# Kernel optimization log

Hardware: AMD Instinct MI355X
Metric: run time of the kernel (lower is better)

Reference implementation:

```python
import jax, jax.numpy as jnp
import numpy as np

B, T, I, H, C = 128, 512, 256, 512, 4


def setup_inputs() -> dict:
    key = jax.random.key(0)
    ks = jax.random.split(key, 11)
    s = lambda fan_in: 1.0 / np.sqrt(fan_in)
    return {
        "x": jax.random.normal(ks[0], (B, T, I), dtype=jnp.float32),
        "W_x1": jax.random.uniform(ks[1], (I, 4 * H), jnp.float32, -s(I), s(I)),
        "b_x1": jax.random.uniform(ks[2], (4 * H,), jnp.float32, -s(I), s(I)),
        "W_h1": jax.random.uniform(ks[3], (H, 4 * H), jnp.float32, -s(H), s(H)),
        "b_h1": jax.random.uniform(ks[4], (4 * H,), jnp.float32, -s(H), s(H)),
        "W_x2": jax.random.uniform(ks[5], (H, 4 * H), jnp.float32, -s(H), s(H)),
        "b_x2": jax.random.uniform(ks[6], (4 * H,), jnp.float32, -s(H), s(H)),
        "W_h2": jax.random.uniform(ks[7], (H, 4 * H), jnp.float32, -s(H), s(H)),
        "b_h2": jax.random.uniform(ks[8], (4 * H,), jnp.float32, -s(H), s(H)),
        "W_head": jax.random.uniform(ks[9], (H, C), jnp.float32, -s(H), s(H)),
        "b_head": jax.random.uniform(ks[10], (C,), jnp.float32, -s(H), s(H)),
    }


def _lstm_layer(x_proj_seq, W_h, b_h, hidden):
    """x_proj_seq: [T, B, 4H] precomputed input projection (incl. x bias).
    Returns full hidden sequence [T, B, H] and final (h, c)."""
    def step(carry, xp_t):
        h, c = carry
        gates = xp_t + h @ W_h + b_h  # [B, 4H]
        i_t, f_t, g_t, o_t = jnp.split(gates, 4, axis=-1)
        i_t = jax.nn.sigmoid(i_t)
        f_t = jax.nn.sigmoid(f_t)
        g_t = jnp.tanh(g_t)
        o_t = jax.nn.sigmoid(o_t)
        c_t = f_t * c + i_t * g_t
        h_t = o_t * jnp.tanh(c_t)
        return (h_t, c_t), h_t

    batch = x_proj_seq.shape[1]
    init = (jnp.zeros((batch, hidden), x_proj_seq.dtype),
            jnp.zeros((batch, hidden), x_proj_seq.dtype))
    (h_T, c_T), h_seq = jax.lax.scan(step, init, x_proj_seq)
    return h_seq, h_T


def reference(x, W_x1, b_x1, W_h1, b_h1, W_x2, b_x2, W_h2, b_h2, W_head, b_head):
    H_ = W_h1.shape[0]
    # Precompute input projections for all timesteps as one big GEMM per layer.
    xp1 = jnp.einsum('bti,ig->tbg', x, W_x1) + b_x1  # [T, B, 4H]
    h1_seq, _ = _lstm_layer(xp1, W_h1, b_h1, H_)      # [T, B, H]
    xp2 = jnp.einsum('tbh,hg->tbg', h1_seq, W_x2) + b_x2
    _, h2_T = _lstm_layer(xp2, W_h2, b_h2, H_)        # [B, H]
    return h2_T @ W_head + b_head                     # [B, C]
```

## Files before the change

### kernel.cpp

```cpp
#include <hip/hip_runtime.h>
#include <cstddef>

#define Bb 128
#define Tt 512
#define Ii 256
#define Hh 512
#define G4c 2048
#define BHc (Bb * Hh)
#define FSTRIDE 32

typedef float    f32x4 __attribute__((ext_vector_type(4)));
typedef _Float16 f16x8 __attribute__((ext_vector_type(8)));
typedef unsigned int u32x4 __attribute__((ext_vector_type(4)));

#define OFF_WT1 0u
#define OFF_WT2 3145728u
#define OFF_BC1 7340032u
#define OFF_BC2 7348224u
#define OFF_H1  7356416u
#define OFF_H2  7749632u
#define OFF_FLG 8011776u
#define OFF_END 8028160u

__device__ __forceinline__ float sigm(float x)  { return 1.0f / (1.0f + __expf(-x)); }
__device__ __forceinline__ float tanhf_(float x){ return 1.0f - 2.0f / (1.0f + __expf(2.0f * x)); }

__device__ __forceinline__ void ld_g_f16x8_sc(f16x8& dst, const _Float16* p) {
  asm volatile("global_load_dwordx4 %0, %1, off sc0 sc1"
               : "=v"(dst) : "v"(p) : "memory");
}
__device__ __forceinline__ void ld_g_f32x4(f32x4& dst, const float* p) {
  asm volatile("global_load_dwordx4 %0, %1, off" : "=v"(dst) : "v"(p) : "memory");
}
__device__ __forceinline__ void st_g_f16_sc(_Float16* p, _Float16 v) {
  unsigned u = (unsigned)__builtin_bit_cast(unsigned short, v);
  asm volatile("global_store_short %0, %1, off sc0 sc1" :: "v"(p), "v"(u) : "memory");
}
__device__ __forceinline__ void wait_vm0() {
  asm volatile("s_waitcnt vmcnt(0)" ::: "memory");
}

__device__ __forceinline__ void poll2(unsigned* base, int tid,
                                      unsigned tgtA, unsigned tgtB) {
  if (tid < 64) {
    const unsigned tgt = (tid < 32) ? tgtA : tgtB;
    unsigned* p = base + (size_t)tid * FSTRIDE;
    unsigned v;
    do {
      v = __hip_atomic_load(p, __ATOMIC_RELAXED, __HIP_MEMORY_SCOPE_AGENT);
    } while (__any(v < tgt));
  }
  __syncthreads();
}

__device__ __forceinline__ void publish(unsigned* myflag, int tid, unsigned val) {
  wait_vm0();
  __syncthreads();
  if (tid == 0)
    __hip_atomic_store(myflag, val, __ATOMIC_RELAXED, __HIP_MEMORY_SCOPE_AGENT);
}

__global__ void init_weights(const float* __restrict__ Wx1, const float* __restrict__ Wh1,
                             const float* __restrict__ bx1, const float* __restrict__ bh1,
                             const float* __restrict__ Wx2, const float* __restrict__ Wh2,
                             const float* __restrict__ bx2, const float* __restrict__ bh2,
                             _Float16* __restrict__ Wt1, _Float16* __restrict__ Wt2,
                             float* __restrict__ bc1, float* __restrict__ bc2) {
  const int b = blockIdx.x;
  const int layer = b >> 11;
  const int jb = (b >> 6) & 31;
  const int ln = b & 63;
  const int t  = threadIdx.x;
  const int ks = t >> 3;
  const int i  = t & 7;
  const int k  = (ks << 5) + ((ln >> 4) << 3) + i;
  if (layer == 0) {
    if (ln == 0 && t < 16) {
      #pragma unroll
      for (int g = 0; g < 4; ++g) {
        const int gc = (g << 9) + (jb << 4) + t;
        bc1[gc] = bx1[gc] + bh1[gc];
      }
    }
    if (ks < 24) {
      #pragma unroll
      for (int g = 0; g < 4; ++g) {
        const int gc = (g << 9) + (jb << 4) + (ln & 15);
        const float v = (k < Ii) ? Wx1[k * G4c + gc] : Wh1[(k - Ii) * G4c + gc];
        Wt1[((((size_t)jb * 24 + ks) * 4 + g) * 64 + ln) * 8 + i] = (_Float16)v;
      }
    }
  } else {
    if (ln == 0 && t < 16) {
      #pragma unroll
      for (int g = 0; g < 4; ++g) {
        const int gc = (g << 9) + (jb << 4) + t;
        bc2[gc] = bx2[gc] + bh2[gc];
      }
    }
    #pragma unroll
    for (int g = 0; g < 4; ++g) {
      const int gc = (g << 9) + (jb << 4) + (ln & 15);
      const float v = (k < Hh) ? Wx2[k * G4c + gc] : Wh2[(k - Hh) * G4c + gc];
      Wt2[((((size_t)jb * 32 + ks) * 4 + g) * 64 + ln) * 8 + i] = (_Float16)v;
    }
  }
}

__global__ void zero_ws(u32x4* p, int n) {
  const int i = blockIdx.x * blockDim.x + threadIdx.x;
  if (i < n) p[i] = (u32x4){0u, 0u, 0u, 0u};
}

__global__ __launch_bounds__(256, 1) void lstm_main(
    const float* __restrict__ x,
    const _Float16* __restrict__ Wt1, const _Float16* __restrict__ Wt2,
    const float* __restrict__ bc1, const float* __restrict__ bc2,
    _Float16* h1buf, _Float16* h2buf, unsigned* flags,
    const float* __restrict__ Whead, const float* __restrict__ bhead,
    float* __restrict__ out)
{
  extern __shared__ char smem[];

  const int tid  = threadIdx.x;
  const int lane = tid & 63;
  const int wv   = tid >> 6;
  const int bid  = blockIdx.x;
  const int layer = bid >> 6;
  const int blkL  = bid & 63;
  const int jb = blkL >> 1;
  const int rh = blkL & 1;
  const int j0 = jb << 4;

  unsigned* grp = flags + (size_t)(rh << 6) * FSTRIDE;
  unsigned* myflag = grp + (size_t)((layer << 5) + jb) * FSTRIDE;

  {
    const int elems16 = layer ? (131072 / 16) : (98304 / 16);
    const u32x4* src = (const u32x4*)((layer ? Wt2 : Wt1)
                                      + (size_t)jb * (layer ? 65536 : 49152));
    u32x4* dst = (u32x4*)smem;
    for (int i = tid; i < elems16; i += 256) dst[i] = src[i];
  }
  __syncthreads();

  const int c15 = lane & 15;
  const int kg  = lane >> 4;
  const int arow  = (rh << 6) + (wv << 4) + c15;
  const int wrow0 = (rh << 6) + (wv << 4) + (kg << 2);

  const float* bc = layer ? bc2 : bc1;
  const float bias0 = bc[        j0 + c15];
  const float bias1 = bc[ 512 +  j0 + c15];
  const float bias2 = bc[1024 +  j0 + c15];
  const float bias3 = bc[1536 +  j0 + c15];

  const int lb = lane << 4;

  f32x4 cst = {0.f, 0.f, 0.f, 0.f};

  int m3w = 0;
  int m3r = 2;

  for (int e = 0; e <= Tt; ++e) {
    if (layer == 0) {
      if (e >= Tt) break;
      f32x4 xf[16];
      const float* xp = x + (size_t)arow * (Tt * Ii) + (size_t)e * Ii + (kg << 3);
      #pragma unroll
      for (int ks = 0; ks < 8; ++ks) {
        ld_g_f32x4(xf[2*ks],   xp + (ks << 5));
        ld_g_f32x4(xf[2*ks+1], xp + (ks << 5) + 4);
      }
      poll2(grp, tid, (unsigned)e, e ? (unsigned)(e - 1) : 0u);
      f16x8 af[24];
      const _Float16* hp = h1buf + (size_t)m3r * BHc + arow * Hh + (kg << 3);
      #pragma unroll
      for (int ks = 0; ks < 16; ++ks)
        ld_g_f16x8_sc(af[8 + ks], hp + (ks << 5));
      wait_vm0();
      __builtin_amdgcn_sched_barrier(0);
      #pragma unroll
      for (int ks = 0; ks < 8; ++ks) {
        f16x8 v;
        v[0] = (_Float16)xf[2*ks][0]; v[1] = (_Float16)xf[2*ks][1];
        v[2] = (_Float16)xf[2*ks][2]; v[3] = (_Float16)xf[2*ks][3];
        v[4] = (_Float16)xf[2*ks+1][0]; v[5] = (_Float16)xf[2*ks+1][1];
        v[6] = (_Float16)xf[2*ks+1][2]; v[7] = (_Float16)xf[2*ks+1][3];
        af[ks] = v;
      }
      f32x4 acc0 = {0.f,0.f,0.f,0.f}, acc1 = {0.f,0.f,0.f,0.f};
      f32x4 acc2 = {0.f,0.f,0.f,0.f}, acc3 = {0.f,0.f,0.f,0.f};
      #pragma unroll
      for (int ks = 0; ks < 24; ++ks) {
        const char* bp = smem + (ks << 12) + lb;
        acc0 = __builtin_amdgcn_mfma_f32_16x16x32_f16(af[ks], *(const f16x8*)(bp       ), acc0, 0, 0, 0);
        acc1 = __builtin_amdgcn_mfma_f32_16x16x32_f16(af[ks], *(const f16x8*)(bp + 1024), acc1, 0, 0, 0);
        acc2 = __builtin_amdgcn_mfma_f32_16x16x32_f16(af[ks], *(const f16x8*)(bp + 2048), acc2, 0, 0, 0);
        acc3 = __builtin_amdgcn_mfma_f32_16x16x32_f16(af[ks], *(const f16x8*)(bp + 3072), acc3, 0, 0, 0);
      }
      float hout[4];
      #pragma unroll
      for (int r = 0; r < 4; ++r) {
        const float iv = sigm(acc0[r] + bias0);
        const float fv = sigm(acc1[r] + bias1);
        const float gv = tanhf_(acc2[r] + bias2);
        const float ov = sigm(acc3[r] + bias3);
        const float cv = fv * cst[r] + iv * gv;
        cst[r] = cv;
        hout[r] = ov * tanhf_(cv);
      }
      _Float16* hw = h1buf + (size_t)m3w * BHc;
      #pragma unroll
      for (int r = 0; r < 4; ++r)
        st_g_f16_sc(hw + (size_t)(wrow0 + r) * Hh + j0 + c15, (_Float16)hout[r]);
      publish(myflag, tid, (unsigned)(e + 1));
    } else {
      if (e == 0) {
        publish(myflag, tid, 1u);
      } else {
        poll2(grp, tid, (unsigned)e, (unsigned)e);
        f16x8 af[32];
        const _Float16* h1p = h1buf + (size_t)m3r * BHc + arow * Hh + (kg << 3);
        const _Float16* h2p = h2buf + (size_t)(e & 1) * BHc + arow * Hh + (kg << 3);
        #pragma unroll
        for (int ks = 0; ks < 16; ++ks)
          ld_g_f16x8_sc(af[ks], h1p + (ks << 5));
        #pragma unroll
        for (int ks = 0; ks < 16; ++ks)
          ld_g_f16x8_sc(af[16 + ks], h2p + (ks << 5));
        wait_vm0();
        __builtin_amdgcn_sched_barrier(0);
        f32x4 acc0 = {0.f,0.f,0.f,0.f}, acc1 = {0.f,0.f,0.f,0.f};
        f32x4 acc2 = {0.f,0.f,0.f,0.f}, acc3 = {0.f,0.f,0.f,0.f};
        #pragma unroll
        for (int ks = 0; ks < 32; ++ks) {
          const char* bp = smem + (ks << 12) + lb;
          acc0 = __builtin_amdgcn_mfma_f32_16x16x32_f16(af[ks], *(const f16x8*)(bp       ), acc0, 0, 0, 0);
          acc1 = __builtin_amdgcn_mfma_f32_16x16x32_f16(af[ks], *(const f16x8*)(bp + 1024), acc1, 0, 0, 0);
          acc2 = __builtin_amdgcn_mfma_f32_16x16x32_f16(af[ks], *(const f16x8*)(bp + 2048), acc2, 0, 0, 0);
          acc3 = __builtin_amdgcn_mfma_f32_16x16x32_f16(af[ks], *(const f16x8*)(bp + 3072), acc3, 0, 0, 0);
        }
        float hout[4];
        #pragma unroll
        for (int r = 0; r < 4; ++r) {
          const float iv = sigm(acc0[r] + bias0);
          const float fv = sigm(acc1[r] + bias1);
          const float gv = tanhf_(acc2[r] + bias2);
          const float ov = sigm(acc3[r] + bias3);
          const float cv = fv * cst[r] + iv * gv;
          cst[r] = cv;
          hout[r] = ov * tanhf_(cv);
        }
        _Float16* hw = h2buf + (size_t)((e + 1) & 1) * BHc;
        #pragma unroll
        for (int r = 0; r < 4; ++r)
          st_g_f16_sc(hw + (size_t)(wrow0 + r) * Hh + j0 + c15, (_Float16)hout[r]);
        publish(myflag, tid, (unsigned)(e + 1));
      }
    }
    m3w = (m3w + 1 == 3) ? 0 : m3w + 1;
    m3r = (m3r + 1 == 3) ? 0 : m3r + 1;
  }

  if (layer == 1 && jb == 0) {
    poll2(grp, tid, 0u, 513u);
    const int b_ = (rh << 6) + (tid >> 2);
    const int cc = tid & 3;
    const _Float16* hr = h2buf + BHc + (size_t)b_ * Hh;
    float s = bhead[cc];
    #pragma unroll
    for (int half = 0; half < 2; ++half) {
      f16x8 hv[32];
      #pragma unroll
      for (int kk = 0; kk < 32; ++kk)
        ld_g_f16x8_sc(hv[kk], hr + (half << 8) + (kk << 3));
      wait_vm0();
      #pragma unroll
      for (int kk = 0; kk < 32; ++kk) {
        const int k = (half << 8) + (kk << 3);
        #pragma unroll
        for (int j = 0; j < 8; ++j)
          s += (float)hv[kk][j] * Whead[(k + j) * 4 + cc];
      }
    }
    out[b_ * 4 + cc] = s;
  }
}

extern "C" void kernel_launch(void* const* d_in, const int* in_sizes, int n_in,
                              void* d_out, int out_size, void* d_ws, size_t ws_size,
                              hipStream_t stream) {
  const float* x   = (const float*)d_in[0];
  const float* Wx1 = (const float*)d_in[1];
  const float* bx1 = (const float*)d_in[2];
  const float* Wh1 = (const float*)d_in[3];
  const float* bh1 = (const float*)d_in[4];
  const float* Wx2 = (const float*)d_in[5];
  const float* bx2 = (const float*)d_in[6];
  const float* Wh2 = (const float*)d_in[7];
  const float* bh2 = (const float*)d_in[8];
  const float* Whd = (const float*)d_in[9];
  const float* bhd = (const float*)d_in[10];

  char* ws = (char*)d_ws;
  _Float16* Wt1 = (_Float16*)(ws + OFF_WT1);
  _Float16* Wt2 = (_Float16*)(ws + OFF_WT2);
  float* bc1 = (float*)(ws + OFF_BC1);
  float* bc2 = (float*)(ws + OFF_BC2);
  _Float16* h1b = (_Float16*)(ws + OFF_H1);
  _Float16* h2b = (_Float16*)(ws + OFF_H2);
  unsigned* flg = (unsigned*)(ws + OFF_FLG);
  float* out = (float*)d_out;

  init_weights<<<4096, 256, 0, stream>>>(Wx1, Wh1, bx1, bh1, Wx2, Wh2, bx2, bh2,
                                         Wt1, Wt2, bc1, bc2);
  {
    u32x4* zp = (u32x4*)(ws + OFF_H1);
    const int n = (int)((OFF_END - OFF_H1) / 16);
    zero_ws<<<(n + 255) / 256, 256, 0, stream>>>(zp, n);
  }
  (void)hipFuncSetAttribute((const void*)lstm_main,
                            hipFuncAttributeMaxDynamicSharedMemorySize, 131072);
  void* args[] = {(void*)&x, (void*)&Wt1, (void*)&Wt2, (void*)&bc1, (void*)&bc2,
                  (void*)&h1b, (void*)&h2b, (void*)&flg,
                  (void*)&Whd, (void*)&bhd, (void*)&out};
  (void)hipLaunchCooperativeKernel((const void*)lstm_main, dim3(128), dim3(256),
                                   args, 131072, stream);
}
```

Before: 3.983 ms.

## Decouple LSTM layer sync with per-layer flags, progress counters and 4-deep h1 ring

Replaces the combined 64-flag poll, where each block waited on all blocks of both layers, with a poll on its own layer's 32 flags plus one peer-progress counter published by the jb==0 block. The h1 buffer ring grows from 3 to 4 slots, so layer 0 may run up to two steps ahead of layer 1 instead of one. This is meant to cut the coupling stalls between the two layer pipelines. It adds an extra atomic progress store per step and more workspace, and correctness now relies on the ring depth matching the slack allowed by the progress counter.

```diff
diff --git a/kernel.cpp b/kernel.cpp
--- a/kernel.cpp
+++ b/kernel.cpp
@@ -18,9 +18,10 @@
 #define OFF_BC1 7340032u
 #define OFF_BC2 7348224u
 #define OFF_H1  7356416u
-#define OFF_H2  7749632u
-#define OFF_FLG 8011776u
-#define OFF_END 8028160u
+#define OFF_H2  7880704u
+#define OFF_FLG 8142848u
+#define OFF_PRG 8159232u
+#define OFF_END 8159744u
 
 __device__ __forceinline__ float sigm(float x)  { return 1.0f / (1.0f + __expf(-x)); }
 __device__ __forceinline__ float tanhf_(float x){ return 1.0f - 2.0f / (1.0f + __expf(2.0f * x)); }
@@ -40,11 +41,11 @@
   asm volatile("s_waitcnt vmcnt(0)" ::: "memory");
 }
 
-__device__ __forceinline__ void poll2(unsigned* base, int tid,
-                                      unsigned tgtA, unsigned tgtB) {
+__device__ __forceinline__ void pollstep(unsigned* grpL, unsigned* peer, int tid,
+                                         unsigned tl, unsigned tp) {
   if (tid < 64) {
-    const unsigned tgt = (tid < 32) ? tgtA : tgtB;
-    unsigned* p = base + (size_t)tid * FSTRIDE;
+    const unsigned tgt = (tid < 32) ? tl : tp;
+    const unsigned* p = (tid < 32) ? grpL + (size_t)tid * FSTRIDE : peer;
     unsigned v;
     do {
       v = __hip_atomic_load(p, __ATOMIC_RELAXED, __HIP_MEMORY_SCOPE_AGENT);
@@ -116,7 +117,7 @@
     const float* __restrict__ x,
     const _Float16* __restrict__ Wt1, const _Float16* __restrict__ Wt2,
     const float* __restrict__ bc1, const float* __restrict__ bc2,
-    _Float16* h1buf, _Float16* h2buf, unsigned* flags,
+    _Float16* h1buf, _Float16* h2buf, unsigned* flags, unsigned* prg,
     const float* __restrict__ Whead, const float* __restrict__ bhead,
     float* __restrict__ out)
 {
@@ -132,8 +133,10 @@
   const int rh = blkL & 1;
   const int j0 = jb << 4;
 
-  unsigned* grp = flags + (size_t)(rh << 6) * FSTRIDE;
-  unsigned* myflag = grp + (size_t)((layer << 5) + jb) * FSTRIDE;
+  unsigned* grpL   = flags + (size_t)((rh << 6) + (layer << 5)) * FSTRIDE;
+  unsigned* myflag = grpL + (size_t)jb * FSTRIDE;
+  unsigned* ownp   = prg + (size_t)((rh << 1) | layer) * FSTRIDE;
+  unsigned* peer   = prg + (size_t)((rh << 1) | (1 - layer)) * FSTRIDE;
 
   {
     const int elems16 = layer ? (131072 / 16) : (98304 / 16);
@@ -159,9 +162,6 @@
 
   f32x4 cst = {0.f, 0.f, 0.f, 0.f};
 
-  int m3w = 0;
-  int m3r = 2;
-
   for (int e = 0; e <= Tt; ++e) {
     if (layer == 0) {
       if (e >= Tt) break;
@@ -172,9 +172,11 @@
         ld_g_f32x4(xf[2*ks],   xp + (ks << 5));
         ld_g_f32x4(xf[2*ks+1], xp + (ks << 5) + 4);
       }
-      poll2(grp, tid, (unsigned)e, e ? (unsigned)(e - 1) : 0u);
+      pollstep(grpL, peer, tid, (unsigned)e, (e >= 2) ? (unsigned)(e - 2) : 0u);
+      if (jb == 0 && tid == 0)
+        __hip_atomic_store(ownp, (unsigned)e, __ATOMIC_RELAXED, __HIP_MEMORY_SCOPE_AGENT);
       f16x8 af[24];
-      const _Float16* hp = h1buf + (size_t)m3r * BHc + arow * Hh + (kg << 3);
+      const _Float16* hp = h1buf + (size_t)((e - 1) & 3) * BHc + arow * Hh + (kg << 3);
       #pragma unroll
       for (int ks = 0; ks < 16; ++ks)
         ld_g_f16x8_sc(af[8 + ks], hp + (ks << 5));
@@ -210,7 +212,7 @@
         cst[r] = cv;
         hout[r] = ov * tanhf_(cv);
       }
-      _Float16* hw = h1buf + (size_t)m3w * BHc;
+      _Float16* hw = h1buf + (size_t)(e & 3) * BHc;
       #pragma unroll
       for (int r = 0; r < 4; ++r)
         st_g_f16_sc(hw + (size_t)(wrow0 + r) * Hh + j0 + c15, (_Float16)hout[r]);
@@ -219,9 +221,11 @@
       if (e == 0) {
         publish(myflag, tid, 1u);
       } else {
-        poll2(grp, tid, (unsigned)e, (unsigned)e);
+        pollstep(grpL, peer, tid, (unsigned)e, (unsigned)e);
+        if (jb == 0 && tid == 0)
+          __hip_atomic_store(ownp, (unsigned)e, __ATOMIC_RELAXED, __HIP_MEMORY_SCOPE_AGENT);
         f16x8 af[32];
-        const _Float16* h1p = h1buf + (size_t)m3r * BHc + arow * Hh + (kg << 3);
+        const _Float16* h1p = h1buf + (size_t)((e - 1) & 3) * BHc + arow * Hh + (kg << 3);
         const _Float16* h2p = h2buf + (size_t)(e & 1) * BHc + arow * Hh + (kg << 3);
         #pragma unroll
         for (int ks = 0; ks < 16; ++ks)
@@ -259,12 +263,16 @@
         publish(myflag, tid, (unsigned)(e + 1));
       }
     }
-    m3w = (m3w + 1 == 3) ? 0 : m3w + 1;
-    m3r = (m3r + 1 == 3) ? 0 : m3r + 1;
-  }
-
-  if (layer == 1 && jb == 0) {
-    poll2(grp, tid, 0u, 513u);
+  }
+
+  if (layer == 0) {
+    if (jb == 0) {
+      pollstep(grpL, peer, tid, (unsigned)Tt, 0u);
+      if (tid == 0)
+        __hip_atomic_store(ownp, (unsigned)Tt, __ATOMIC_RELAXED, __HIP_MEMORY_SCOPE_AGENT);
+    }
+  } else if (jb == 0) {
+    pollstep(grpL, peer, tid, (unsigned)(Tt + 1), 0u);
     const int b_ = (rh << 6) + (tid >> 2);
     const int cc = tid & 3;
     const _Float16* hr = h2buf + BHc + (size_t)b_ * Hh;
@@ -311,6 +319,7 @@
   _Float16* h1b = (_Float16*)(ws + OFF_H1);
   _Float16* h2b = (_Float16*)(ws + OFF_H2);
   unsigned* flg = (unsigned*)(ws + OFF_FLG);
+  unsigned* prg = (unsigned*)(ws + OFF_PRG);
   float* out = (float*)d_out;
 
   init_weights<<<4096, 256, 0, stream>>>(Wx1, Wh1, bx1, bh1, Wx2, Wh2, bx2, bh2,
@@ -323,7 +332,7 @@
   (void)hipFuncSetAttribute((const void*)lstm_main,
                             hipFuncAttributeMaxDynamicSharedMemorySize, 131072);
   void* args[] = {(void*)&x, (void*)&Wt1, (void*)&Wt2, (void*)&bc1, (void*)&bc2,
-                  (void*)&h1b, (void*)&h2b, (void*)&flg,
+                  (void*)&h1b, (void*)&h2b, (void*)&flg, (void*)&prg,
                   (void*)&Whd, (void*)&bhd, (void*)&out};
   (void)hipLaunchCooperativeKernel((const void*)lstm_main, dim3(128), dim3(256),
                                    args, 131072, stream);
```

Measured after the change: 4.045 ms. About the same (+1.6%).

## Split batch into four independent groups across 256 blocks with pairwise flag sync

Applied to the files above, without the earlier changes.

The grid grows from 128 to 256 blocks. Each block now handles 32 batch rows instead of 64, and the four gate MFMAs are split across wave pairs, with an LDS exchange before the gate nonlinearities. Synchronisation becomes per-group between own and peer flags for each batch half, instead of one combined group. Each layer-0 step now issues 24 MFMA pairs rather than 24×4 per wave, and h stores are packed into dwords. This shortens the serial per-step critical path, at the cost of an extra LDS round-trip, extra syncthreads, and a spin cap that can silently abort.

```diff
diff --git a/kernel.cpp b/kernel.cpp
--- a/kernel.cpp
+++ b/kernel.cpp
@@ -1,13 +1,12 @@
 #include <hip/hip_runtime.h>
 #include <cstddef>
 
-#define Bb 128
 #define Tt 512
 #define Ii 256
 #define Hh 512
 #define G4c 2048
-#define BHc (Bb * Hh)
 #define FSTRIDE 32
+#define SPIN_CAP 50000000
 
 typedef float    f32x4 __attribute__((ext_vector_type(4)));
 typedef _Float16 f16x8 __attribute__((ext_vector_type(8)));
@@ -18,9 +17,11 @@
 #define OFF_BC1 7340032u
 #define OFF_BC2 7348224u
 #define OFF_H1  7356416u
-#define OFF_H2  7749632u
-#define OFF_FLG 8011776u
-#define OFF_END 8028160u
+#define OFF_H2  7618560u
+#define OFF_FLG 7880704u
+#define OFF_END 7913472u
+
+#define MFMA(a,b,c) __builtin_amdgcn_mfma_f32_16x16x32_f16((a),(b),(c),0,0,0)
 
 __device__ __forceinline__ float sigm(float x)  { return 1.0f / (1.0f + __expf(-x)); }
 __device__ __forceinline__ float tanhf_(float x){ return 1.0f - 2.0f / (1.0f + __expf(2.0f * x)); }
@@ -32,22 +33,29 @@
 __device__ __forceinline__ void ld_g_f32x4(f32x4& dst, const float* p) {
   asm volatile("global_load_dwordx4 %0, %1, off" : "=v"(dst) : "v"(p) : "memory");
 }
-__device__ __forceinline__ void st_g_f16_sc(_Float16* p, _Float16 v) {
-  unsigned u = (unsigned)__builtin_bit_cast(unsigned short, v);
-  asm volatile("global_store_short %0, %1, off sc0 sc1" :: "v"(p), "v"(u) : "memory");
+__device__ __forceinline__ void st_g_u32_sc(void* p, unsigned v) {
+  asm volatile("global_store_dword %0, %1, off sc0 sc1" :: "v"(p), "v"(v) : "memory");
 }
 __device__ __forceinline__ void wait_vm0() {
   asm volatile("s_waitcnt vmcnt(0)" ::: "memory");
 }
-
-__device__ __forceinline__ void poll2(unsigned* base, int tid,
-                                      unsigned tgtA, unsigned tgtB) {
+__device__ __forceinline__ unsigned packh(float a, float b) {
+  unsigned short ua = __builtin_bit_cast(unsigned short, (_Float16)a);
+  unsigned short ub = __builtin_bit_cast(unsigned short, (_Float16)b);
+  return (unsigned)ua | ((unsigned)ub << 16);
+}
+
+__device__ __forceinline__ void pollstep(unsigned* own, unsigned* peer,
+                                         int* s_abort, int tid,
+                                         unsigned tl, unsigned tp) {
   if (tid < 64) {
-    const unsigned tgt = (tid < 32) ? tgtA : tgtB;
-    unsigned* p = base + (size_t)tid * FSTRIDE;
-    unsigned v;
+    const unsigned tgt = (tid < 32) ? tl : tp;
+    const unsigned* p = (tid < 32) ? own + (size_t)tid * FSTRIDE
+                                   : peer + (size_t)(tid - 32) * FSTRIDE;
+    unsigned v; int guard = 0;
     do {
       v = __hip_atomic_load(p, __ATOMIC_RELAXED, __HIP_MEMORY_SCOPE_AGENT);
+      if (++guard > SPIN_CAP) { if (tid == 0) *s_abort = 1; break; }
     } while (__any(v < tgt));
   }
   __syncthreads();
@@ -121,19 +129,23 @@
     float* __restrict__ out)
 {
   extern __shared__ char smem[];
+  __shared__ f32x4 gxs[512];
+  __shared__ int s_abort;
 
   const int tid  = threadIdx.x;
   const int lane = tid & 63;
   const int wv   = tid >> 6;
   const int bid  = blockIdx.x;
-  const int layer = bid >> 6;
-  const int blkL  = bid & 63;
-  const int jb = blkL >> 1;
-  const int rh = blkL & 1;
+  const int g    = bid >> 5;
+  const int jb   = bid & 31;
+  const int layer = g & 1;
+  const int rh    = g >> 1;
   const int j0 = jb << 4;
-
-  unsigned* grp = flags + (size_t)(rh << 6) * FSTRIDE;
-  unsigned* myflag = grp + (size_t)((layer << 5) + jb) * FSTRIDE;
+  if (tid == 0) s_abort = 0;
+
+  unsigned* own  = flags + (size_t)(g << 5) * FSTRIDE;
+  unsigned* peer = flags + (size_t)((g ^ 1) << 5) * FSTRIDE;
+  unsigned* myfl = own + (size_t)jb * FSTRIDE;
 
   {
     const int elems16 = layer ? (131072 / 16) : (98304 / 16);
@@ -144,40 +156,56 @@
   }
   __syncthreads();
 
+  const int rt  = wv & 1;
+  const int u   = wv >> 1;
   const int c15 = lane & 15;
   const int kg  = lane >> 4;
-  const int arow  = (rh << 6) + (wv << 4) + c15;
-  const int wrow0 = (rh << 6) + (wv << 4) + (kg << 2);
-
-  const float* bc = layer ? bc2 : bc1;
-  const float bias0 = bc[        j0 + c15];
-  const float bias1 = bc[ 512 +  j0 + c15];
-  const float bias2 = bc[1024 +  j0 + c15];
-  const float bias3 = bc[1536 +  j0 + c15];
-
-  const int lb = lane << 4;
-
-  f32x4 cst = {0.f, 0.f, 0.f, 0.f};
-
-  int m3w = 0;
-  int m3r = 2;
-
-  for (int e = 0; e <= Tt; ++e) {
+  const int lb  = lane << 4;
+
+  _Float16* h1b = h1buf + (size_t)rh * 2 * 16384;
+  _Float16* h2b = h2buf + (size_t)rh * 2 * 16384;
+  const int browA = rh * 32 + rt * 16 + c15;
+  const int arowl = rt * 16 + c15;
+
+  const int erow = tid >> 3;
+  const int col2 = (tid & 7) << 1;
+  const int ert = erow >> 4, er15 = erow & 15;
+  const float* bcL = layer ? bc2 : bc1;
+  float bi_[4][2];
+  #pragma unroll
+  for (int gg = 0; gg < 4; ++gg) {
+    bi_[gg][0] = bcL[(gg << 9) + j0 + col2];
+    bi_[gg][1] = bcL[(gg << 9) + j0 + col2 + 1];
+  }
+  float cst0 = 0.f, cst1 = 0.f;
+  const size_t eo = (size_t)erow * 512 + j0 + col2;
+
+  for (int t = 0; t < Tt; ++t) {
+    f32x4 a0 = {0.f,0.f,0.f,0.f}, a1 = {0.f,0.f,0.f,0.f};
     if (layer == 0) {
-      if (e >= Tt) break;
       f32x4 xf[16];
-      const float* xp = x + (size_t)arow * (Tt * Ii) + (size_t)e * Ii + (kg << 3);
+      const float* xp = x + ((size_t)browA * Tt + t) * Ii + (kg << 3);
       #pragma unroll
       for (int ks = 0; ks < 8; ++ks) {
-        ld_g_f32x4(xf[2*ks],   xp + (ks << 5));
-        ld_g_f32x4(xf[2*ks+1], xp + (ks << 5) + 4);
-      }
-      poll2(grp, tid, (unsigned)e, e ? (unsigned)(e - 1) : 0u);
+        ld_g_f32x4(xf[2 * ks],     xp + (ks << 5));
+        ld_g_f32x4(xf[2 * ks + 1], xp + (ks << 5) + 4);
+      }
+      pollstep(own, peer, &s_abort, tid,
+               (unsigned)t, (t >= 1) ? (unsigned)(t - 1) : 0u);
+      if (s_abort) return;
       f16x8 af[24];
-      const _Float16* hp = h1buf + (size_t)m3r * BHc + arow * Hh + (kg << 3);
-      #pragma unroll
-      for (int ks = 0; ks < 16; ++ks)
-        ld_g_f16x8_sc(af[8 + ks], hp + (ks << 5));
+      if (t > 0) {
+        const _Float16* hp = h1b + (size_t)((t - 1) & 1) * 16384
+                             + (size_t)arowl * 512 + (kg << 3);
+        #pragma unroll
+        for (int ks = 0; ks < 16; ++ks)
+          ld_g_f16x8_sc(af[8 + ks], hp + (ks << 5));
+      } else {
+        #pragma unroll
+        for (int ks = 0; ks < 16; ++ks)
+          #pragma unroll
+          for (int q = 0; q < 8; ++q) af[8 + ks][q] = (_Float16)0.f;
+      }
       wait_vm0();
       __builtin_amdgcn_sched_barrier(0);
       #pragma unroll
@@ -189,102 +217,94 @@
         v[6] = (_Float16)xf[2*ks+1][2]; v[7] = (_Float16)xf[2*ks+1][3];
         af[ks] = v;
       }
-      f32x4 acc0 = {0.f,0.f,0.f,0.f}, acc1 = {0.f,0.f,0.f,0.f};
-      f32x4 acc2 = {0.f,0.f,0.f,0.f}, acc3 = {0.f,0.f,0.f,0.f};
       #pragma unroll
       for (int ks = 0; ks < 24; ++ks) {
-        const char* bp = smem + (ks << 12) + lb;
-        acc0 = __builtin_amdgcn_mfma_f32_16x16x32_f16(af[ks], *(const f16x8*)(bp       ), acc0, 0, 0, 0);
-        acc1 = __builtin_amdgcn_mfma_f32_16x16x32_f16(af[ks], *(const f16x8*)(bp + 1024), acc1, 0, 0, 0);
-        acc2 = __builtin_amdgcn_mfma_f32_16x16x32_f16(af[ks], *(const f16x8*)(bp + 2048), acc2, 0, 0, 0);
-        acc3 = __builtin_amdgcn_mfma_f32_16x16x32_f16(af[ks], *(const f16x8*)(bp + 3072), acc3, 0, 0, 0);
-      }
-      float hout[4];
-      #pragma unroll
-      for (int r = 0; r < 4; ++r) {
-        const float iv = sigm(acc0[r] + bias0);
-        const float fv = sigm(acc1[r] + bias1);
-        const float gv = tanhf_(acc2[r] + bias2);
-        const float ov = sigm(acc3[r] + bias3);
-        const float cv = fv * cst[r] + iv * gv;
-        cst[r] = cv;
-        hout[r] = ov * tanhf_(cv);
-      }
-      _Float16* hw = h1buf + (size_t)m3w * BHc;
-      #pragma unroll
-      for (int r = 0; r < 4; ++r)
-        st_g_f16_sc(hw + (size_t)(wrow0 + r) * Hh + j0 + c15, (_Float16)hout[r]);
-      publish(myflag, tid, (unsigned)(e + 1));
+        const char* bp = smem + (ks << 12) + (u << 11) + lb;
+        a0 = MFMA(af[ks], *(const f16x8*)(bp), a0);
+        a1 = MFMA(af[ks], *(const f16x8*)(bp + 1024), a1);
+      }
     } else {
-      if (e == 0) {
-        publish(myflag, tid, 1u);
-      } else {
-        poll2(grp, tid, (unsigned)e, (unsigned)e);
-        f16x8 af[32];
-        const _Float16* h1p = h1buf + (size_t)m3r * BHc + arow * Hh + (kg << 3);
-        const _Float16* h2p = h2buf + (size_t)(e & 1) * BHc + arow * Hh + (kg << 3);
-        #pragma unroll
-        for (int ks = 0; ks < 16; ++ks)
-          ld_g_f16x8_sc(af[ks], h1p + (ks << 5));
+      pollstep(own, peer, &s_abort, tid, (unsigned)t, (unsigned)(t + 1));
+      if (s_abort) return;
+      f16x8 af[32];
+      const _Float16* h1p = h1b + (size_t)(t & 1) * 16384
+                            + (size_t)arowl * 512 + (kg << 3);
+      #pragma unroll
+      for (int ks = 0; ks < 16; ++ks)
+        ld_g_f16x8_sc(af[ks], h1p + (ks << 5));
+      if (t > 0) {
+        const _Float16* h2p = h2b + (size_t)((t - 1) & 1) * 16384
+                              + (size_t)arowl * 512 + (kg << 3);
         #pragma unroll
         for (int ks = 0; ks < 16; ++ks)
           ld_g_f16x8_sc(af[16 + ks], h2p + (ks << 5));
+      } else {
+        #pragma unroll
+        for (int ks = 0; ks < 16; ++ks)
+          #pragma unroll
+          for (int q = 0; q < 8; ++q) af[16 + ks][q] = (_Float16)0.f;
+      }
+      wait_vm0();
+      __builtin_amdgcn_sched_barrier(0);
+      #pragma unroll
+      for (int ks = 0; ks < 32; ++ks) {
+        const char* bp = smem + (ks << 12) + (u << 11) + lb;
+        a0 = MFMA(af[ks], *(const f16x8*)(bp), a0);
+        a1 = MFMA(af[ks], *(const f16x8*)(bp + 1024), a1);
+      }
+    }
+
+    gxs[((rt * 4 + 2 * u)     * 16 + c15) * 4 + kg] = a0;
+    gxs[((rt * 4 + 2 * u + 1) * 16 + c15) * 4 + kg] = a1;
+    __syncthreads();
+
+    const float* gb = (const float*)gxs;
+    const int f0 = (ert * 4) * 256 + col2 * 16 + er15;
+    const int f1 = f0 + 16;
+    const float i0 = sigm (gb[f0      ] + bi_[0][0]);
+    const float fv0= sigm (gb[f0 + 256] + bi_[1][0]);
+    const float g0 = tanhf_(gb[f0 + 512] + bi_[2][0]);
+    const float o0 = sigm (gb[f0 + 768] + bi_[3][0]);
+    const float i1 = sigm (gb[f1      ] + bi_[0][1]);
+    const float fv1= sigm (gb[f1 + 256] + bi_[1][1]);
+    const float g1 = tanhf_(gb[f1 + 512] + bi_[2][1]);
+    const float o1 = sigm (gb[f1 + 768] + bi_[3][1]);
+    const float cv0 = fv0 * cst0 + i0 * g0; cst0 = cv0;
+    const float cv1 = fv1 * cst1 + i1 * g1; cst1 = cv1;
+    const unsigned hu = packh(o0 * tanhf_(cv0), o1 * tanhf_(cv1));
+
+    _Float16* hw = (layer == 0) ? (h1b + (size_t)(t & 1) * 16384)
+                                : (h2b + (size_t)(t & 1) * 16384);
+    st_g_u32_sc((char*)(hw + eo), hu);
+    __syncthreads();
+    publish(myfl, tid, (unsigned)(t + 1));
+  }
+
+  if (layer == 1 && jb == 0) {
+    pollstep(own, peer, &s_abort, tid, (unsigned)Tt, 0u);
+    if (s_abort) return;
+    if (tid < 128) {
+      const int row = tid >> 2;
+      const int cc = tid & 3;
+      const _Float16* hr = h2b + 16384 + (size_t)row * 512;
+      float s = bhead[cc];
+      #pragma unroll
+      for (int half = 0; half < 4; ++half) {
+        f16x8 hv[16];
+        #pragma unroll
+        for (int j = 0; j < 16; ++j)
+          ld_g_f16x8_sc(hv[j], hr + (half << 7) + (j << 3));
         wait_vm0();
-        __builtin_amdgcn_sched_barrier(0);
-        f32x4 acc0 = {0.f,0.f,0.f,0.f}, acc1 = {0.f,0.f,0.f,0.f};
-        f32x4 acc2 = {0.f,0.f,0.f,0.f}, acc3 = {0.f,0.f,0.f,0.f};
-        #pragma unroll
-        for (int ks = 0; ks < 32; ++ks) {
-          const char* bp = smem + (ks << 12) + lb;
-          acc0 = __builtin_amdgcn_mfma_f32_16x16x32_f16(af[ks], *(const f16x8*)(bp       ), acc0, 0, 0, 0);
-          acc1 = __builtin_amdgcn_mfma_f32_16x16x32_f16(af[ks], *(const f16x8*)(bp + 1024), acc1, 0, 0, 0);
-          acc2 = __builtin_amdgcn_mfma_f32_16x16x32_f16(af[ks], *(const f16x8*)(bp + 2048), acc2, 0, 0, 0);
-          acc3 = __builtin_amdgcn_mfma_f32_16x16x32_f16(af[ks], *(const f16x8*)(bp + 3072), acc3, 0, 0, 0);
+        #pragma unroll
+        for (int j = 0; j < 16; ++j) {
+          const int k = (half << 7) + (j << 3);
+          #pragma unroll
+          for (int e = 0; e < 8; ++e)
+            s += (float)hv[j][e] * Whead[(k + e) * 4 + cc];
         }
-        float hout[4];
-        #pragma unroll
-        for (int r = 0; r < 4; ++r) {
-          const float iv = sigm(acc0[r] + bias0);
-          const float fv = sigm(acc1[r] + bias1);
-          const float gv = tanhf_(acc2[r] + bias2);
-          const float ov = sigm(acc3[r] + bias3);
-          const float cv = fv * cst[r] + iv * gv;
-          cst[r] = cv;
-          hout[r] = ov * tanhf_(cv);
-        }
-        _Float16* hw = h2buf + (size_t)((e + 1) & 1) * BHc;
-        #pragma unroll
-        for (int r = 0; r < 4; ++r)
-          st_g_f16_sc(hw + (size_t)(wrow0 + r) * Hh + j0 + c15, (_Float16)hout[r]);
-        publish(myflag, tid, (unsigned)(e + 1));
-      }
-    }
-    m3w = (m3w + 1 == 3) ? 0 : m3w + 1;
-    m3r = (m3r + 1 == 3) ? 0 : m3r + 1;
-  }
-
-  if (layer == 1 && jb == 0) {
-    poll2(grp, tid, 0u, 513u);
-    const int b_ = (rh << 6) + (tid >> 2);
-    const int cc = tid & 3;
-    const _Float16* hr = h2buf + BHc + (size_t)b_ * Hh;
-    float s = bhead[cc];
-    #pragma unroll
-    for (int half = 0; half < 2; ++half) {
-      f16x8 hv[32];
-      #pragma unroll
-      for (int kk = 0; kk < 32; ++kk)
-        ld_g_f16x8_sc(hv[kk], hr + (half << 8) + (kk << 3));
-      wait_vm0();
-      #pragma unroll
-      for (int kk = 0; kk < 32; ++kk) {
-        const int k = (half << 8) + (kk << 3);
-        #pragma unroll
-        for (int j = 0; j < 8; ++j)
-          s += (float)hv[kk][j] * Whead[(k + j) * 4 + cc];
-      }
-    }
-    out[b_ * 4 + cc] = s;
+      }
+      out[(rh * 32 + row) * 4 + cc] = s;
+    }
   }
 }
 
@@ -325,6 +345,6 @@
   void* args[] = {(void*)&x, (void*)&Wt1, (void*)&Wt2, (void*)&bc1, (void*)&bc2,
                   (void*)&h1b, (void*)&h2b, (void*)&flg,
                   (void*)&Whd, (void*)&bhd, (void*)&out};
-  (void)hipLaunchCooperativeKernel((const void*)lstm_main, dim3(128), dim3(256),
+  (void)hipLaunchCooperativeKernel((const void*)lstm_main, dim3(256), dim3(256),
                                    args, 131072, stream);
 }
```

Result: faster. 3.555 ms (median of 2 runs) (-10.7%).
